# Optimization experiments

Measured on AMD Instinct MI355X. Metric: run time of the kernel, lower is better.

## Reference

```python
import jax, jax.numpy as jnp
import numpy as np

H = 8192  # hidden width; structure = [42, H, H, 8]


def setup_inputs() -> dict:
    key = jax.random.key(0)
    ks = jax.random.split(key, 6)
    # Connect-4 board: 42 cells with values 0 (empty), 1, 2 (players)
    state = jax.random.randint(ks[0], (42,), 0, 3).astype(jnp.float32)
    state = state.at[0].set(0.0)  # guarantee at least one legal column
    s = 0.02
    W1 = jax.random.normal(ks[1], (42, H), jnp.float32) * s
    b1 = jnp.zeros((H,), jnp.float32)
    W2 = jax.random.normal(ks[2], (H, H), jnp.float32) * s
    b2 = jnp.zeros((H,), jnp.float32)
    W3 = jax.random.normal(ks[3], (H, 8), jnp.float32) * s
    b3 = jnp.zeros((8,), jnp.float32)
    return {"state": state, "W1": W1, "b1": b1, "W2": W2, "b2": b2,
            "W3": W3, "b3": b3}


def reference(state, W1, b1, W2, b2, W3, b3):
    x = state.reshape(1, 42)
    x = jax.nn.relu(x @ W1 + b1)          # [1, H]
    x = jax.nn.relu(x @ W2 + b2)          # [1, H]
    pen = x @ W3 + b3                      # [1, 8] = 7 move logits + value
    value = pen[:, -1]                     # [1]
    # mask(state): column i legal iff top-row cell state[i] == 0
    legal = state[:7] == 0                 # [7] bool
    logits = pen[0, :7]                    # [7]
    masked = jnp.where(legal, logits, -jnp.inf)
    p = jax.nn.softmax(masked)             # softmax over legal entries only
    # scatter reduced distribution back into fixed [7,1] slots
    distribution = jnp.where(legal, p, 0.0).reshape(7, 1)
    return (value, distribution)
```

## Files before the change

kernel.cpp:

```cpp
#include <hip/hip_runtime.h>
#include <math.h>

#define H 8192
#define NSPLIT 64
#define ROWS_PER_SPLIT (H / NSPLIT)
#define JCHUNK 1024


__global__ void k1_h1(const float* __restrict__ state,
                      const float* __restrict__ W1,
                      const float* __restrict__ b1,
                      float* __restrict__ h1) {
    int j = (blockIdx.x * blockDim.x + threadIdx.x) * 4;
    float4 acc = *(const float4*)(b1 + j);
    #pragma unroll 6
    for (int i = 0; i < 42; ++i) {
        float s = state[i];
        float4 w = *(const float4*)(W1 + (size_t)i * H + j);
        acc.x = fmaf(s, w.x, acc.x);
        acc.y = fmaf(s, w.y, acc.y);
        acc.z = fmaf(s, w.z, acc.z);
        acc.w = fmaf(s, w.w, acc.w);
    }
    acc.x = fmaxf(acc.x, 0.0f);
    acc.y = fmaxf(acc.y, 0.0f);
    acc.z = fmaxf(acc.z, 0.0f);
    acc.w = fmaxf(acc.w, 0.0f);
    *(float4*)(h1 + j) = acc;
}

__global__ void k2_partial(const float* __restrict__ W2,
                           const float* __restrict__ h1,
                           float* __restrict__ partial) {
    int j  = blockIdx.x * JCHUNK + threadIdx.x * 4;
    int i0 = blockIdx.y * ROWS_PER_SPLIT;
    float4 acc = make_float4(0.f, 0.f, 0.f, 0.f);
    const float* wp = W2 + (size_t)i0 * H + j;
    const float* hp = h1 + i0;
    #pragma unroll 16
    for (int ii = 0; ii < ROWS_PER_SPLIT; ++ii) {
        float s  = hp[ii];
        float4 w = *(const float4*)wp;
        wp += H;
        acc.x = fmaf(s, w.x, acc.x);
        acc.y = fmaf(s, w.y, acc.y);
        acc.z = fmaf(s, w.z, acc.z);
        acc.w = fmaf(s, w.w, acc.w);
    }
    *(float4*)(partial + (size_t)blockIdx.y * H + j) = acc;
}

__global__ void k3_reduce(const float* __restrict__ partial,
                          const float* __restrict__ b2,
                          float* __restrict__ h2) {
    int j = blockIdx.x * blockDim.x + threadIdx.x;
    float acc = b2[j];
    #pragma unroll 8
    for (int s = 0; s < NSPLIT; ++s) {
        acc += partial[(size_t)s * H + j];
    }
    h2[j] = fmaxf(acc, 0.0f);
}

__global__ void k4_final(const float* __restrict__ h2,
                         const float* __restrict__ W3,
                         const float* __restrict__ b3,
                         const float* __restrict__ state,
                         float* __restrict__ out) {
    float acc[8];
    #pragma unroll
    for (int k = 0; k < 8; ++k) acc[k] = 0.0f;

    #pragma unroll
    for (int r = 0; r < H / 1024; ++r) {
        int j = threadIdx.x + r * 1024;
        float h = h2[j];
        float4 w0 = *(const float4*)(W3 + (size_t)j * 8);
        float4 w1 = *(const float4*)(W3 + (size_t)j * 8 + 4);
        acc[0] = fmaf(h, w0.x, acc[0]);
        acc[1] = fmaf(h, w0.y, acc[1]);
        acc[2] = fmaf(h, w0.z, acc[2]);
        acc[3] = fmaf(h, w0.w, acc[3]);
        acc[4] = fmaf(h, w1.x, acc[4]);
        acc[5] = fmaf(h, w1.y, acc[5]);
        acc[6] = fmaf(h, w1.z, acc[6]);
        acc[7] = fmaf(h, w1.w, acc[7]);
    }

    #pragma unroll
    for (int off = 32; off > 0; off >>= 1) {
        #pragma unroll
        for (int k = 0; k < 8; ++k)
            acc[k] += __shfl_down(acc[k], off);
    }

    __shared__ float red[16][8];
    int wave = threadIdx.x >> 6;
    int lane = threadIdx.x & 63;
    if (lane == 0) {
        #pragma unroll
        for (int k = 0; k < 8; ++k) red[wave][k] = acc[k];
    }
    __syncthreads();

    if (threadIdx.x == 0) {
        float pen[8];
        #pragma unroll
        for (int k = 0; k < 8; ++k) {
            float s = b3[k];
            for (int w = 0; w < 16; ++w) s += red[w][k];
            pen[k] = s;
        }
        out[0] = pen[7];
        bool legal[7];
        float m = -INFINITY;
        for (int i = 0; i < 7; ++i) {
            legal[i] = (state[i] == 0.0f);
            if (legal[i] && pen[i] > m) m = pen[i];
        }
        float e[7];
        float sum = 0.0f;
        for (int i = 0; i < 7; ++i) {
            e[i] = legal[i] ? expf(pen[i] - m) : 0.0f;
            sum += e[i];
        }
        float inv = 1.0f / sum;
        for (int i = 0; i < 7; ++i) out[1 + i] = e[i] * inv;
    }
}

extern "C" void kernel_launch(void* const* d_in, const int* in_sizes, int n_in,
                              void* d_out, int out_size, void* d_ws, size_t ws_size,
                              hipStream_t stream) {
    const float* state = (const float*)d_in[0];
    const float* W1    = (const float*)d_in[1];
    const float* b1    = (const float*)d_in[2];
    const float* W2    = (const float*)d_in[3];
    const float* b2    = (const float*)d_in[4];
    const float* W3    = (const float*)d_in[5];
    const float* b3    = (const float*)d_in[6];
    float* out = (float*)d_out;

    float* ws      = (float*)d_ws;
    float* h1      = ws;
    float* h2      = ws + H;
    float* partial = ws + 2 * H;

    hipLaunchKernelGGL(k1_h1, dim3(H / 1024), dim3(256), 0, stream, state, W1, b1, h1);
    hipLaunchKernelGGL(k2_partial, dim3(H / JCHUNK, NSPLIT), dim3(256), 0, stream, W2, h1, partial);
    hipLaunchKernelGGL(k3_reduce, dim3(H / 256), dim3(256), 0, stream, partial, b2, h2);
    hipLaunchKernelGGL(k4_final, dim3(1), dim3(1024), 0, stream, h2, W3, b3, state, out);
}
```

Measured before the change: 391.6 us.

## Compact nonzero ReLU activations to skip zero rows of W2

The first layer now compacts the positive post-ReLU activations of each 1024-column segment into value/row lists in shared memory. The main matvec then reads only the W2 rows whose input activation is nonzero, split evenly across 64 slices, instead of streaming all of W2. The bandwidth-bound second layer should then read roughly half as much data. The third-layer reduction is folded into the reduce kernel using wave shuffles plus global atomics, leaving a tiny final softmax kernel. This adds data-dependent row gathers in an unordered sequence and makes float summation order nondeterministic.

```diff
diff --git a/kernel.cpp b/kernel.cpp
--- a/kernel.cpp
+++ b/kernel.cpp
@@ -3,15 +3,31 @@
 
 #define H 8192
 #define NSPLIT 64
-#define ROWS_PER_SPLIT (H / NSPLIT)
-#define JCHUNK 1024
+#define NSEG 8
+#define SEGCOLS 1024
 
+#define WS_VALS 0
+#define WS_ROWS 8192
+#define WS_CNT 16384
+#define WS_PEN 16392
+#define WS_PARTIAL 16400
 
 __global__ void k1_h1(const float* __restrict__ state,
                       const float* __restrict__ W1,
                       const float* __restrict__ b1,
-                      float* __restrict__ h1) {
-    int j = (blockIdx.x * blockDim.x + threadIdx.x) * 4;
+                      float* __restrict__ vals,
+                      int* __restrict__ rows,
+                      int* __restrict__ cnt,
+                      float* __restrict__ pen) {
+    __shared__ float sv[SEGCOLS];
+    __shared__ int   sr[SEGCOLS];
+    __shared__ int   scnt;
+    int tid = threadIdx.x;
+    if (tid == 0) scnt = 0;
+    if (blockIdx.x == 0 && tid < 8) pen[tid] = 0.0f;
+    __syncthreads();
+
+    int j = blockIdx.x * SEGCOLS + tid * 4;
     float4 acc = *(const float4*)(b1 + j);
     #pragma unroll 6
     for (int i = 0; i < 42; ++i) {
@@ -22,106 +38,106 @@
         acc.z = fmaf(s, w.z, acc.z);
         acc.w = fmaf(s, w.w, acc.w);
     }
-    acc.x = fmaxf(acc.x, 0.0f);
-    acc.y = fmaxf(acc.y, 0.0f);
-    acc.z = fmaxf(acc.z, 0.0f);
-    acc.w = fmaxf(acc.w, 0.0f);
-    *(float4*)(h1 + j) = acc;
+    float v[4] = { fmaxf(acc.x, 0.f), fmaxf(acc.y, 0.f),
+                   fmaxf(acc.z, 0.f), fmaxf(acc.w, 0.f) };
+    #pragma unroll
+    for (int c = 0; c < 4; ++c) {
+        if (v[c] > 0.0f) {
+            int p = atomicAdd(&scnt, 1);
+            sv[p] = v[c];
+            sr[p] = j + c;
+        }
+    }
+    __syncthreads();
+    int n = scnt;
+    if (tid == 0) cnt[blockIdx.x] = n;
+    int base = blockIdx.x * SEGCOLS;
+    for (int p = tid; p < n; p += blockDim.x) {
+        vals[base + p] = sv[p];
+        rows[base + p] = sr[p];
+    }
 }
 
 __global__ void k2_partial(const float* __restrict__ W2,
-                           const float* __restrict__ h1,
+                           const float* __restrict__ vals,
+                           const int* __restrict__ rows,
+                           const int* __restrict__ cnt,
                            float* __restrict__ partial) {
-    int j  = blockIdx.x * JCHUNK + threadIdx.x * 4;
-    int i0 = blockIdx.y * ROWS_PER_SPLIT;
+    int j = blockIdx.x * SEGCOLS + threadIdx.x * 4;
+
+    int c[NSEG], pre[NSEG + 1];
+    pre[0] = 0;
+    #pragma unroll
+    for (int b = 0; b < NSEG; ++b) { c[b] = cnt[b]; pre[b + 1] = pre[b] + c[b]; }
+    int total = pre[NSEG];
+    int chunk = (total + NSPLIT - 1) / NSPLIT;
+    int glo = blockIdx.y * chunk;
+    int ghi = min(glo + chunk, total);
+
     float4 acc = make_float4(0.f, 0.f, 0.f, 0.f);
-    const float* wp = W2 + (size_t)i0 * H + j;
-    const float* hp = h1 + i0;
-    #pragma unroll 16
-    for (int ii = 0; ii < ROWS_PER_SPLIT; ++ii) {
-        float s  = hp[ii];
-        float4 w = *(const float4*)wp;
-        wp += H;
-        acc.x = fmaf(s, w.x, acc.x);
-        acc.y = fmaf(s, w.y, acc.y);
-        acc.z = fmaf(s, w.z, acc.z);
-        acc.w = fmaf(s, w.w, acc.w);
+    #pragma unroll
+    for (int b = 0; b < NSEG; ++b) {
+        int lo = max(glo, pre[b]);
+        int hi = min(ghi, pre[b] + c[b]);
+        int off = b * SEGCOLS - pre[b];
+        #pragma unroll 4
+        for (int p = lo; p < hi; ++p) {
+            float s = vals[off + p];
+            int   r = rows[off + p];
+            float4 w = *(const float4*)(W2 + (size_t)r * H + j);
+            acc.x = fmaf(s, w.x, acc.x);
+            acc.y = fmaf(s, w.y, acc.y);
+            acc.z = fmaf(s, w.z, acc.z);
+            acc.w = fmaf(s, w.w, acc.w);
+        }
     }
     *(float4*)(partial + (size_t)blockIdx.y * H + j) = acc;
 }
 
 __global__ void k3_reduce(const float* __restrict__ partial,
                           const float* __restrict__ b2,
-                          float* __restrict__ h2) {
+                          const float* __restrict__ W3,
+                          float* __restrict__ pen) {
     int j = blockIdx.x * blockDim.x + threadIdx.x;
     float acc = b2[j];
     #pragma unroll 8
-    for (int s = 0; s < NSPLIT; ++s) {
-        acc += partial[(size_t)s * H + j];
-    }
-    h2[j] = fmaxf(acc, 0.0f);
-}
+    for (int s = 0; s < NSPLIT; ++s) acc += partial[(size_t)s * H + j];
+    float h = fmaxf(acc, 0.0f);
 
-__global__ void k4_final(const float* __restrict__ h2,
-                         const float* __restrict__ W3,
-                         const float* __restrict__ b3,
-                         const float* __restrict__ state,
-                         float* __restrict__ out) {
-    float acc[8];
-    #pragma unroll
-    for (int k = 0; k < 8; ++k) acc[k] = 0.0f;
-
-    #pragma unroll
-    for (int r = 0; r < H / 1024; ++r) {
-        int j = threadIdx.x + r * 1024;
-        float h = h2[j];
-        float4 w0 = *(const float4*)(W3 + (size_t)j * 8);
-        float4 w1 = *(const float4*)(W3 + (size_t)j * 8 + 4);
-        acc[0] = fmaf(h, w0.x, acc[0]);
-        acc[1] = fmaf(h, w0.y, acc[1]);
-        acc[2] = fmaf(h, w0.z, acc[2]);
-        acc[3] = fmaf(h, w0.w, acc[3]);
-        acc[4] = fmaf(h, w1.x, acc[4]);
-        acc[5] = fmaf(h, w1.y, acc[5]);
-        acc[6] = fmaf(h, w1.z, acc[6]);
-        acc[7] = fmaf(h, w1.w, acc[7]);
-    }
+    float4 w0 = *(const float4*)(W3 + (size_t)j * 8);
+    float4 w1 = *(const float4*)(W3 + (size_t)j * 8 + 4);
+    float a[8] = { h * w0.x, h * w0.y, h * w0.z, h * w0.w,
+                   h * w1.x, h * w1.y, h * w1.z, h * w1.w };
 
     #pragma unroll
     for (int off = 32; off > 0; off >>= 1) {
         #pragma unroll
-        for (int k = 0; k < 8; ++k)
-            acc[k] += __shfl_down(acc[k], off);
+        for (int k = 0; k < 8; ++k) a[k] += __shfl_down(a[k], off);
     }
+    if ((threadIdx.x & 63) == 0) {
+        #pragma unroll
+        for (int k = 0; k < 8; ++k) atomicAdd(&pen[k], a[k]);
+    }
+}
 
-    __shared__ float red[16][8];
-    int wave = threadIdx.x >> 6;
-    int lane = threadIdx.x & 63;
-    if (lane == 0) {
+__global__ void k4_final(const float* __restrict__ pen,
+                         const float* __restrict__ b3,
+                         const float* __restrict__ state,
+                         float* __restrict__ out) {
+    if (threadIdx.x == 0) {
+        float p8[8];
         #pragma unroll
-        for (int k = 0; k < 8; ++k) red[wave][k] = acc[k];
-    }
-    __syncthreads();
-
-    if (threadIdx.x == 0) {
-        float pen[8];
-        #pragma unroll
-        for (int k = 0; k < 8; ++k) {
-            float s = b3[k];
-            for (int w = 0; w < 16; ++w) s += red[w][k];
-            pen[k] = s;
-        }
-        out[0] = pen[7];
+        for (int k = 0; k < 8; ++k) p8[k] = pen[k] + b3[k];
+        out[0] = p8[7];
         bool legal[7];
         float m = -INFINITY;
         for (int i = 0; i < 7; ++i) {
             legal[i] = (state[i] == 0.0f);
-            if (legal[i] && pen[i] > m) m = pen[i];
+            if (legal[i] && p8[i] > m) m = p8[i];
         }
-        float e[7];
-        float sum = 0.0f;
+        float e[7], sum = 0.0f;
         for (int i = 0; i < 7; ++i) {
-            e[i] = legal[i] ? expf(pen[i] - m) : 0.0f;
+            e[i] = legal[i] ? expf(p8[i] - m) : 0.0f;
             sum += e[i];
         }
         float inv = 1.0f / sum;
@@ -142,12 +158,18 @@
     float* out = (float*)d_out;
 
     float* ws      = (float*)d_ws;
-    float* h1      = ws;
-    float* h2      = ws + H;
-    float* partial = ws + 2 * H;
+    float* vals    = ws + WS_VALS;
+    int*   rows    = (int*)(ws + WS_ROWS);
+    int*   cnt     = (int*)(ws + WS_CNT);
+    float* pen     = ws + WS_PEN;
+    float* partial = ws + WS_PARTIAL;
 
-    hipLaunchKernelGGL(k1_h1, dim3(H / 1024), dim3(256), 0, stream, state, W1, b1, h1);
-    hipLaunchKernelGGL(k2_partial, dim3(H / JCHUNK, NSPLIT), dim3(256), 0, stream, W2, h1, partial);
-    hipLaunchKernelGGL(k3_reduce, dim3(H / 256), dim3(256), 0, stream, partial, b2, h2);
-    hipLaunchKernelGGL(k4_final, dim3(1), dim3(1024), 0, stream, h2, W3, b3, state, out);
+    hipLaunchKernelGGL(k1_h1, dim3(NSEG), dim3(256), 0, stream,
+                       state, W1, b1, vals, rows, cnt, pen);
+    hipLaunchKernelGGL(k2_partial, dim3(H / SEGCOLS, NSPLIT), dim3(256), 0, stream,
+                       W2, vals, rows, cnt, partial);
+    hipLaunchKernelGGL(k3_reduce, dim3(H / 256), dim3(256), 0, stream,
+                       partial, b2, W3, pen);
+    hipLaunchKernelGGL(k4_final, dim3(1), dim3(64), 0, stream,
+                       pen, b3, state, out);
 }
```

New measurement: 364.8 us. 1.07x faster.
